# Performance work log

Hardware: AMD Instinct MI355X
Metric: run time of the kernel (lower is better)

The kernel has to match this reference:

```python
import jax, jax.numpy as jnp
import numpy as np

HEADS = 16  # matches init_kwargs


def setup_inputs() -> dict:
    key = jax.random.key(0)
    ks = jax.random.split(key, 9)
    N, L, E, D = 2, 2048, 1024, 64
    return {
        "query": jax.random.normal(ks[0], (N, L, E), dtype=jnp.float32),
        "keys": jax.random.normal(ks[1], (N, L, E), dtype=jnp.float32),
        "values": jax.random.normal(ks[2], (N, L, E), dtype=jnp.float32),
        "masks": jax.random.randint(ks[3], (N, 1, 1, L), 0, 2, dtype=jnp.int32),
        "Wq": jax.random.normal(ks[4], (D, D), dtype=jnp.float32) / np.sqrt(D),
        "Wk": jax.random.normal(ks[5], (D, D), dtype=jnp.float32) / np.sqrt(D),
        "Wv": jax.random.normal(ks[6], (D, D), dtype=jnp.float32) / np.sqrt(D),
        "Wo": jax.random.normal(ks[7], (E, E), dtype=jnp.float32) / np.sqrt(E),
        "bo": jax.random.normal(ks[8], (E,), dtype=jnp.float32),
    }


def reference(query, keys, values, masks, Wq, Wk, Wv, Wo, bo):
    N, Lq, E = query.shape
    Lk = keys.shape[1]
    H = HEADS
    D = E // H
    # split heads: [N, L, H, D]
    q = query.reshape(N, Lq, H, D)
    k = keys.reshape(N, Lk, H, D)
    v = values.reshape(N, Lk, H, D)
    # per-head linear projections (weights shared across heads); Linear: x @ W.T
    q = jnp.einsum("nqhd,ed->nqhe", q, Wq)
    k = jnp.einsum("nkhd,ed->nkhe", k, Wk)
    v = jnp.einsum("nkhd,ed->nkhe", v, Wv)
    # scores [N, H, Lq, Lk]
    scores = jnp.einsum("nqhd,nkhd->nhqk", q, k)
    scores = jnp.where(masks == 0, jnp.float32(-1e20), scores)
    # NOTE: original scales by sqrt(embed_size), not sqrt(head_dim)
    attn = jax.nn.softmax(scores / jnp.sqrt(jnp.float32(E)), axis=3)
    out = jnp.einsum("nhqk,nkhd->nqhd", attn, v).reshape(N, Lq, E)
    return out @ Wo.T + bo
```

## Files before the change

kernel.cpp:

```cpp
#include <hip/hip_runtime.h>


typedef __bf16 bf16_t;
typedef __bf16 bf16x4 __attribute__((ext_vector_type(4)));
typedef __bf16 bf16x8 __attribute__((ext_vector_type(8)));
typedef float f32x4 __attribute__((ext_vector_type(4)));
typedef unsigned int u32x4 __attribute__((ext_vector_type(4)));

#define MFMA16(a, b, c) __builtin_amdgcn_mfma_f32_16x16x32_bf16((a), (b), (c), 0, 0, 0)

#define GLOAD_LDS16(gp, lp)                                              \
    __builtin_amdgcn_global_load_lds(                                    \
        (const __attribute__((address_space(1))) void*)(gp),             \
        (__attribute__((address_space(3))) void*)(lp), 16, 0, 0)

__device__ inline bf16x8 cvt8(const float* __restrict__ p, float scale) {
    f32x4 a = *(const f32x4*)p;
    f32x4 b = *(const f32x4*)(p + 4);
    bf16x8 r;
    r[0] = (bf16_t)(a[0] * scale); r[1] = (bf16_t)(a[1] * scale);
    r[2] = (bf16_t)(a[2] * scale); r[3] = (bf16_t)(a[3] * scale);
    r[4] = (bf16_t)(b[0] * scale); r[5] = (bf16_t)(b[1] * scale);
    r[6] = (bf16_t)(b[2] * scale); r[7] = (bf16_t)(b[3] * scale);
    return r;
}

__device__ inline bf16x8 cvt8s(const f32x4 a, const f32x4 b, float scale) {
    bf16x8 r;
    r[0] = (bf16_t)(a[0] * scale); r[1] = (bf16_t)(a[1] * scale);
    r[2] = (bf16_t)(a[2] * scale); r[3] = (bf16_t)(a[3] * scale);
    r[4] = (bf16_t)(b[0] * scale); r[5] = (bf16_t)(b[1] * scale);
    r[6] = (bf16_t)(b[2] * scale); r[7] = (bf16_t)(b[3] * scale);
    return r;
}

__device__ inline float exp2_fast(float x) {
    float r;
    asm("v_exp_f32 %0, %1" : "=v"(r) : "v"(x));
    return r;
}

__device__ inline unsigned cvt_pk_bf16(float lo, float hi) {
    unsigned r;
    asm("v_cvt_pk_bf16_f32 %0, %1, %2" : "=v"(r) : "v"(lo), "v"(hi));
    return r;
}

__device__ inline void xchg_quads(unsigned &x, unsigned &y) {
    asm("v_permlane32_swap_b32 %0, %1\n\t"
        "v_permlane16_swap_b32 %0, %1"
        : "+v"(x), "+v"(y));
}

__global__ __launch_bounds__(256) void scan_kernel(const int* __restrict__ msk,
                                                   int* __restrict__ excl,
                                                   int* __restrict__ lmap)
{
    __shared__ int wsum[4];
    const int n = blockIdx.x;
    const int t = threadIdx.x, lane = t & 63, w = t >> 6;
    const int* m = msk + n * 2048;
    int* e = excl + n * 2049;
    int* lm = lmap + n * 2048;

    int v[8], s = 0;
    #pragma unroll
    for (int j = 0; j < 8; j++) { v[j] = (m[t * 8 + j] != 0); s += v[j]; }

    int inc = s;
    #pragma unroll
    for (int d = 1; d < 64; d <<= 1) {
        int o = __shfl_up(inc, d);
        if (lane >= d) inc += o;
    }
    if (lane == 63) wsum[w] = inc;
    __syncthreads();
    int off = 0;
    #pragma unroll
    for (int i = 0; i < 4; i++)
        if (i < w) off += wsum[i];

    int a = off + inc - s;
    #pragma unroll
    for (int j = 0; j < 8; j++) {
        e[t * 8 + j] = a;
        if (v[j]) lm[a] = t * 8 + j;
        a += v[j];
    }
    if (t == 255) e[2048] = a;
}

__global__ __launch_bounds__(256) void qkv_proj_kernel(
    const float* __restrict__ qin, const float* __restrict__ kin,
    const float* __restrict__ vin,
    const float* __restrict__ Wq, const float* __restrict__ Wk,
    const float* __restrict__ Wv, const float* __restrict__ Wo,
    const int* __restrict__ excl, const int* __restrict__ lmap,
    bf16_t* __restrict__ qp, bf16_t* __restrict__ kc, bf16_t* __restrict__ vcT,
    bf16_t* __restrict__ Wob)
{
    __shared__ __align__(16) char smem[51200];

    const int t = threadIdx.x;
    const int w = t >> 6, lane = t & 63, quad = lane >> 4, l16 = lane & 15;

    if (blockIdx.y == 3) {
        int idx = blockIdx.x * 1024 + t * 4;
        f32x4 v = *(const f32x4*)&Wo[idx];
        bf16x4 r;
        r[0] = (bf16_t)v[0]; r[1] = (bf16_t)v[1];
        r[2] = (bf16_t)v[2]; r[3] = (bf16_t)v[3];
        *(bf16x4*)&Wob[idx] = r;
        return;
    }

    if (blockIdx.y == 2) {
        bf16_t* Ct = (bf16_t*)smem;
        const int h = blockIdx.x & 15;
        const int ctile = blockIdx.x >> 4;
        const int n = ctile >> 5;
        const int c0 = (ctile & 31) * 64;
        const int Lc = excl[n * 2049 + 2048];
        if (c0 >= Lc) return;

        const int p0 = w * 16 + l16;
        int cs = c0 + p0; if (cs > Lc - 1) cs = Lc - 1;
        const int tg = lmap[n * 2048 + cs];
        const size_t rb = ((size_t)(n * 2048 + tg)) * 1024 + h * 64;

        bf16x8 b0 = cvt8(&vin[rb + quad * 8], 1.0f);
        bf16x8 b1 = cvt8(&vin[rb + 32 + quad * 8], 1.0f);

        #pragma unroll
        for (int nt = 0; nt < 4; nt++) {
            bf16x8 a0 = cvt8(&Wv[(nt * 16 + l16) * 64 + quad * 8], 1.0f);
            bf16x8 a1 = cvt8(&Wv[(nt * 16 + l16) * 64 + 32 + quad * 8], 1.0f);
            f32x4 acc = {0.f, 0.f, 0.f, 0.f};
            acc = MFMA16(a0, b0, acc);
            acc = MFMA16(a1, b1, acc);
            #pragma unroll
            for (int r = 0; r < 4; r++)
                Ct[(nt * 16 + quad * 4 + r) * 72 + w * 16 + l16] = (bf16_t)acc[r];
        }
        __syncthreads();
        const int p = t & 63, rg = t >> 6;
        const int cnt = (Lc - c0 < 64) ? (Lc - c0) : 64;
        if (p < cnt) {
            size_t ob = ((size_t)(n * 16 + h)) * 131072 + c0 + p;
            #pragma unroll
            for (int rr = 0; rr < 16; rr++) {
                int r = rg * 16 + rr;
                vcT[ob + (size_t)r * 2048] = Ct[r * 72 + p];
            }
        }
        return;
    }

    if (blockIdx.x >= 512) return;
    const bool isK = (blockIdx.y == 1);
    const float* x; const float* W; float scale;
    int n = 0, c0 = 0, Lc = 0;
    if (!isK) { x = qin; W = Wq; scale = 0.04508422f; }
    else {
        x = kin; W = Wk; scale = 1.0f;
        n = blockIdx.x >> 8;
        c0 = (blockIdx.x & 255) * 8;
        Lc = excl[n * 2049 + 2048];
        if (c0 >= Lc) return;
    }

    float* Xs = (float*)smem;
    bf16_t* Ct2 = (bf16_t*)(smem + 32768);

    const int g0 = blockIdx.x * 128;

    #pragma unroll
    for (int j = 0; j < 8; j++) {
        int br = w * 32 + j * 4;
        int srow = br + (lane >> 4);
        int scol = ((lane & 15) ^ (srow & 15)) * 4;
        size_t gaddr;
        if (!isK) {
            gaddr = (size_t)(g0 + srow) * 64 + scol;
        } else {
            int csx = c0 + (srow >> 4); if (csx > Lc - 1) csx = Lc - 1;
            int hs = srow & 15;
            int ls = lmap[n * 2048 + csx];
            gaddr = ((size_t)((n * 2048 + ls) * 16 + hs)) * 64 + scol;
        }
        GLOAD_LDS16(&x[gaddr], &Xs[br * 64]);
    }
    __syncthreads();

    const int rbase = w * 32;
    bf16x8 a[2][2];
    #pragma unroll
    for (int qs = 0; qs < 2; qs++) {
        int row = rbase + qs * 16 + l16;
        const char* rowp = (const char*)Xs + (size_t)row * 256;
        int swb = (row & 15) << 4;
        #pragma unroll
        for (int c = 0; c < 2; c++) {
            f32x4 lo = *(const f32x4*)(rowp + ((c * 128 + quad * 32) ^ swb));
            f32x4 hi = *(const f32x4*)(rowp + ((c * 128 + quad * 32 + 16) ^ swb));
            a[qs][c] = cvt8s(lo, hi, scale);
        }
    }

    f32x4 acc[4][2];
    #pragma unroll
    for (int nt = 0; nt < 4; nt++) {
        bf16x8 b0 = cvt8(&W[(nt * 16 + l16) * 64 + quad * 8], 1.0f);
        bf16x8 b1 = cvt8(&W[(nt * 16 + l16) * 64 + 32 + quad * 8], 1.0f);
        #pragma unroll
        for (int qs = 0; qs < 2; qs++) {
            f32x4 z = {0.f, 0.f, 0.f, 0.f};
            z = MFMA16(a[qs][0], b0, z);
            z = MFMA16(a[qs][1], b1, z);
            acc[nt][qs] = z;
        }
    }

    #pragma unroll
    for (int nt = 0; nt < 4; nt++)
        #pragma unroll
        for (int qs = 0; qs < 2; qs++)
            #pragma unroll
            for (int r = 0; r < 4; r++)
                Ct2[(rbase + qs * 16 + quad * 4 + r) * 72 + nt * 16 + l16] = (bf16_t)acc[nt][qs][r];
    __syncthreads();

    #pragma unroll
    for (int it = 0; it < 4; it++) {
        int j = it * 32 + (t >> 3);
        bf16x8 val = *(const bf16x8*)&Ct2[j * 72 + (t & 7) * 8];
        if (isK) {
            int c = c0 + (j >> 4), h2 = j & 15;
            if (c < Lc)
                *(bf16x8*)&kc[(((size_t)(n * 16 + h2)) * 2048 + c) * 64 + (t & 7) * 8] = val;
        } else {
            int g = g0 + j, h2 = g & 15, token = g >> 4;
            int n2 = token >> 11, l = token & 2047;
            *(bf16x8*)&qp[(((size_t)(n2 * 16 + h2)) * 2048 + l) * 64 + (t & 7) * 8] = val;
        }
    }
}

__global__ __launch_bounds__(256) void attn_kernel(
    const bf16_t* __restrict__ qp, const bf16_t* __restrict__ kc,
    const bf16_t* __restrict__ vcT, const int* __restrict__ excl,
    bf16_t* __restrict__ ao)
{
    __shared__ bf16_t Kt[2][128][64];
    __shared__ bf16_t Vt[2][64][128];

    const int t = threadIdx.x;
    const int w = t >> 6, lane = t & 63, quad = lane >> 4, l16 = lane & 15;

    const int flat = blockIdx.x;
    const int xcd = flat & 7, slot = flat >> 3;
    const int nh = xcd * 4 + (slot >> 4), qb = slot & 15;
    const int n = nh >> 4, h = nh & 15;
    const int qbase = qb * 128 + w * 32;
    const size_t nhbase = (size_t)nh * 131072;

    const int Lc = excl[n * 2049 + 2048];
    const int ntiles = (Lc + 127) >> 7;

    const int ksrow = lane >> 3;
    const int kscol = ((lane & 7) ^ (lane >> 3)) * 8;
    const int swr = l16 & 7;
    const int ck0 = (quad ^ swr) * 8;
    const int ck1 = ((quad + 4) ^ swr) * 8;

    bf16x8 aq[2][2];
    #pragma unroll
    for (int qs = 0; qs < 2; qs++)
        #pragma unroll
        for (int c = 0; c < 2; c++)
            aq[qs][c] = *(const bf16x8*)&qp[nhbase + (size_t)(qbase + qs * 16 + l16) * 64 + c * 32 + quad * 8];

    f32x4 o[2][4];
    float lsum[2] = {0.f, 0.f};
    #pragma unroll
    for (int qs = 0; qs < 2; qs++)
        #pragma unroll
        for (int dt = 0; dt < 4; dt++) {
            o[qs][dt][0] = 0.f; o[qs][dt][1] = 0.f; o[qs][dt][2] = 0.f; o[qs][dt][3] = 0.f;
        }

#define STAGE_KV(buf, kn)                                                     \
    {                                                                         \
        _Pragma("unroll")                                                     \
        for (int j = 0; j < 4; j++) {                                         \
            int rb = w * 32 + j * 8;                                          \
            GLOAD_LDS16(&kc[nhbase + (size_t)((kn) + rb + ksrow) * 64 + kscol],\
                        &Kt[buf][rb][0]);                                     \
        }                                                                     \
        _Pragma("unroll")                                                     \
        for (int j = 0; j < 4; j++) {                                         \
            int rb = w * 16 + j * 4;                                          \
            int d = rb + (lane >> 4);                                         \
            int sc = ((lane & 15) ^ (d & 15)) * 8;                            \
            GLOAD_LDS16(&vcT[nhbase + (size_t)d * 2048 + (kn) + sc],          \
                        &Vt[buf][rb][0]);                                     \
        }                                                                     \
    }

    STAGE_KV(0, 0);

    for (int i = 0; i < ntiles; i++) {
        const int cb = i & 1, nb = cb ^ 1;
        const int k0 = i * 128;
        __syncthreads();

        if (i + 1 < ntiles) STAGE_KV(nb, k0 + 128);

        #pragma unroll
        for (int hf = 0; hf < 2; hf++) {
            const int kh = k0 + hf * 64;

            f32x4 st[2][4];
            __builtin_amdgcn_s_setprio(1);
            #pragma unroll
            for (int ct = 0; ct < 4; ct++) {
                bf16x8 kb0 = *(const bf16x8*)&Kt[cb][hf * 64 + ct * 16 + l16][ck0];
                bf16x8 kb1 = *(const bf16x8*)&Kt[cb][hf * 64 + ct * 16 + l16][ck1];
                #pragma unroll
                for (int qs = 0; qs < 2; qs++) {
                    f32x4 acc = {0.f, 0.f, 0.f, 0.f};
                    acc = MFMA16(kb0, aq[qs][0], acc);
                    acc = MFMA16(kb1, aq[qs][1], acc);
                    st[qs][ct] = acc;
                }
            }
            __builtin_amdgcn_s_setprio(0);

            if (kh + 64 <= Lc) {
                #pragma unroll
                for (int qs = 0; qs < 2; qs++)
                    #pragma unroll
                    for (int ct = 0; ct < 4; ct++)
                        #pragma unroll
                        for (int r = 0; r < 4; r++) {
                            float p = exp2_fast(st[qs][ct][r]);
                            lsum[qs] += p;
                            st[qs][ct][r] = p;
                        }
            } else {
                #pragma unroll
                for (int qs = 0; qs < 2; qs++)
                    #pragma unroll
                    for (int ct = 0; ct < 4; ct++)
                        #pragma unroll
                        for (int r = 0; r < 4; r++) {
                            int kk = kh + ct * 16 + quad * 4 + r;
                            float p = (kk < Lc) ? exp2_fast(st[qs][ct][r]) : 0.0f;
                            lsum[qs] += p;
                            st[qs][ct][r] = p;
                        }
            }

            bf16x8 bp[2][2];
            #pragma unroll
            for (int qs = 0; qs < 2; qs++) {
                unsigned u[4][2];
                #pragma unroll
                for (int ct = 0; ct < 4; ct++) {
                    u[ct][0] = cvt_pk_bf16(st[qs][ct][0], st[qs][ct][1]);
                    u[ct][1] = cvt_pk_bf16(st[qs][ct][2], st[qs][ct][3]);
                }
                #pragma unroll
                for (int hh = 0; hh < 2; hh++) {
                    unsigned b0 = u[2 * hh][0], b2 = u[2 * hh + 1][0];
                    xchg_quads(b0, b2);
                    unsigned b1 = u[2 * hh][1], b3 = u[2 * hh + 1][1];
                    xchg_quads(b1, b3);
                    u32x4 q4 = {b0, b1, b2, b3};
                    bp[qs][hh] = __builtin_bit_cast(bf16x8, q4);
                }
            }

            __builtin_amdgcn_s_setprio(1);
            #pragma unroll
            for (int dt = 0; dt < 4; dt++) {
                bf16x8 va0 = *(const bf16x8*)&Vt[cb][dt * 16 + l16][((hf * 8 + quad) ^ l16) * 8];
                bf16x8 va1 = *(const bf16x8*)&Vt[cb][dt * 16 + l16][((hf * 8 + 4 + quad) ^ l16) * 8];
                #pragma unroll
                for (int qs = 0; qs < 2; qs++) {
                    o[qs][dt] = MFMA16(va0, bp[qs][0], o[qs][dt]);
                    o[qs][dt] = MFMA16(va1, bp[qs][1], o[qs][dt]);
                }
            }
            __builtin_amdgcn_s_setprio(0);
        }
    }

    #pragma unroll
    for (int qs = 0; qs < 2; qs++) {
        float v = lsum[qs];
        v += __shfl_xor(v, 16);
        v += __shfl_xor(v, 32);
        float inv = 1.0f / v;
        const int q = qbase + qs * 16 + l16;
        const size_t base = ((size_t)n * 2048 + q) * 1024 + h * 64;
        #pragma unroll
        for (int dt = 0; dt < 4; dt++) {
            bf16x4 ov;
            #pragma unroll
            for (int r = 0; r < 4; r++) ov[r] = (bf16_t)(o[qs][dt][r] * inv);
            *(bf16x4*)&ao[base + dt * 16 + quad * 4] = ov;
        }
    }
}

__global__ __launch_bounds__(256, 2) void out_proj_kernel(
    const bf16_t* __restrict__ X, const bf16_t* __restrict__ Wob,
    const float* __restrict__ bo, float* __restrict__ out)
{
    __shared__ bf16_t Xs[2][128][64];
    __shared__ bf16_t Ws[2][64][64];

    const int t = threadIdx.x;
    const int w = t >> 6, lane = t & 63, quad = lane >> 4, l16 = lane & 15;
    const int Mbase = blockIdx.x * 128;
    const int Nbase = blockIdx.y * 64;
    const int mrow = (w & 1) * 64;
    const int ncol = (w >> 1) * 32;

    const int scol = ((lane & 7) ^ (lane >> 3)) * 8;
    const int swr  = l16 & 7;

    f32x4 acc[4][2];
    #pragma unroll
    for (int mi = 0; mi < 4; mi++)
        #pragma unroll
        for (int ni = 0; ni < 2; ni++) {
            acc[mi][ni][0] = 0.f; acc[mi][ni][1] = 0.f;
            acc[mi][ni][2] = 0.f; acc[mi][ni][3] = 0.f;
        }

    #pragma unroll
    for (int j = 0; j < 4; j++) {
        int br = w * 32 + j * 8;
        GLOAD_LDS16(&X[(size_t)(Mbase + br + (lane >> 3)) * 1024 + scol], &Xs[0][br][0]);
    }
    #pragma unroll
    for (int j = 0; j < 2; j++) {
        int br = w * 16 + j * 8;
        GLOAD_LDS16(&Wob[(size_t)(Nbase + br + (lane >> 3)) * 1024 + scol], &Ws[0][br][0]);
    }

    for (int i = 0; i < 16; i++) {
        const int cb = i & 1, nb = cb ^ 1;
        __syncthreads();

        if (i < 15) {
            const int kn = (i + 1) * 64;
            #pragma unroll
            for (int j = 0; j < 4; j++) {
                int br = w * 32 + j * 8;
                GLOAD_LDS16(&X[(size_t)(Mbase + br + (lane >> 3)) * 1024 + kn + scol],
                            &Xs[nb][br][0]);
            }
            #pragma unroll
            for (int j = 0; j < 2; j++) {
                int br = w * 16 + j * 8;
                GLOAD_LDS16(&Wob[(size_t)(Nbase + br + (lane >> 3)) * 1024 + kn + scol],
                            &Ws[nb][br][0]);
            }
        }

        #pragma unroll
        for (int c = 0; c < 2; c++) {
            bf16x8 bfr[2];
            #pragma unroll
            for (int ni = 0; ni < 2; ni++)
                bfr[ni] = *(const bf16x8*)&Ws[cb][ncol + ni * 16 + l16][((c * 4 + quad) ^ swr) * 8];
            #pragma unroll
            for (int mi = 0; mi < 4; mi++) {
                bf16x8 afr = *(const bf16x8*)&Xs[cb][mrow + mi * 16 + l16][((c * 4 + quad) ^ swr) * 8];
                #pragma unroll
                for (int ni = 0; ni < 2; ni++)
                    acc[mi][ni] = MFMA16(afr, bfr[ni], acc[mi][ni]);
            }
        }
    }

    #pragma unroll
    for (int ni = 0; ni < 2; ni++) {
        float b = bo[Nbase + ncol + ni * 16 + l16];
        #pragma unroll
        for (int mi = 0; mi < 4; mi++) {
            #pragma unroll
            for (int r = 0; r < 4; r++) {
                int row = Mbase + mrow + mi * 16 + quad * 4 + r;
                out[(size_t)row * 1024 + Nbase + ncol + ni * 16 + l16] = acc[mi][ni][r] + b;
            }
        }
    }
}

extern "C" void kernel_launch(void* const* d_in, const int* in_sizes, int n_in,
                              void* d_out, int out_size, void* d_ws, size_t ws_size,
                              hipStream_t stream)
{
    const float* qin = (const float*)d_in[0];
    const float* kin = (const float*)d_in[1];
    const float* vin = (const float*)d_in[2];
    const int*   msk = (const int*)d_in[3];
    const float* Wq  = (const float*)d_in[4];
    const float* Wk  = (const float*)d_in[5];
    const float* Wv  = (const float*)d_in[6];
    const float* Wo  = (const float*)d_in[7];
    const float* bo  = (const float*)d_in[8];
    float* out = (float*)d_out;

    bf16_t* ws  = (bf16_t*)d_ws;
    bf16_t* qp  = ws;
    bf16_t* kc  = ws + 4194304;
    bf16_t* vcT = ws + 8388608;
    bf16_t* ao  = ws + 12582912;
    bf16_t* Wob = ws + 16777216;
    int* excl   = (int*)(ws + 17825792);
    int* lmap   = excl + 4100;

    scan_kernel<<<2, 256, 0, stream>>>(msk, excl, lmap);
    qkv_proj_kernel<<<dim3(1024, 4), 256, 0, stream>>>(qin, kin, vin, Wq, Wk, Wv, Wo,
                                                        excl, lmap, qp, kc, vcT, Wob);
    attn_kernel<<<dim3(512), 256, 0, stream>>>(qp, kc, vcT, excl, ao);
    out_proj_kernel<<<dim3(32, 16), 256, 0, stream>>>(ao, Wob, bo, out);
}
```

Measured before the change: 167.0 us.

## Pre-convert projection weights to bf16 and widen out-proj N tile

Converts Wq (with the softmax scale folded in), Wk and Wv to bf16 once, in extra blocks of the scan kernel. The QKV projection blocks then load bf16 weights directly instead of converting fp32 in every block, and the Q activation scaling is removed. The output projection tile grows from 128x64 to 128x128 per block, which halves the grid and doubles the accumulators per thread. That improves operand reuse but costs more registers and LDS, and leaves fewer blocks to fill the GPU.

```diff
diff --git a/kernel.cpp b/kernel.cpp
--- a/kernel.cpp
+++ b/kernel.cpp
@@ -14,23 +14,23 @@
         (const __attribute__((address_space(1))) void*)(gp),             \
         (__attribute__((address_space(3))) void*)(lp), 16, 0, 0)
 
-__device__ inline bf16x8 cvt8(const float* __restrict__ p, float scale) {
+__device__ inline bf16x8 cvt8(const float* __restrict__ p) {
     f32x4 a = *(const f32x4*)p;
     f32x4 b = *(const f32x4*)(p + 4);
     bf16x8 r;
-    r[0] = (bf16_t)(a[0] * scale); r[1] = (bf16_t)(a[1] * scale);
-    r[2] = (bf16_t)(a[2] * scale); r[3] = (bf16_t)(a[3] * scale);
-    r[4] = (bf16_t)(b[0] * scale); r[5] = (bf16_t)(b[1] * scale);
-    r[6] = (bf16_t)(b[2] * scale); r[7] = (bf16_t)(b[3] * scale);
+    r[0] = (bf16_t)a[0]; r[1] = (bf16_t)a[1];
+    r[2] = (bf16_t)a[2]; r[3] = (bf16_t)a[3];
+    r[4] = (bf16_t)b[0]; r[5] = (bf16_t)b[1];
+    r[6] = (bf16_t)b[2]; r[7] = (bf16_t)b[3];
     return r;
 }
 
-__device__ inline bf16x8 cvt8s(const f32x4 a, const f32x4 b, float scale) {
+__device__ inline bf16x8 cvt8s(const f32x4 a, const f32x4 b) {
     bf16x8 r;
-    r[0] = (bf16_t)(a[0] * scale); r[1] = (bf16_t)(a[1] * scale);
-    r[2] = (bf16_t)(a[2] * scale); r[3] = (bf16_t)(a[3] * scale);
-    r[4] = (bf16_t)(b[0] * scale); r[5] = (bf16_t)(b[1] * scale);
-    r[6] = (bf16_t)(b[2] * scale); r[7] = (bf16_t)(b[3] * scale);
+    r[0] = (bf16_t)a[0]; r[1] = (bf16_t)a[1];
+    r[2] = (bf16_t)a[2]; r[3] = (bf16_t)a[3];
+    r[4] = (bf16_t)b[0]; r[5] = (bf16_t)b[1];
+    r[6] = (bf16_t)b[2]; r[7] = (bf16_t)b[3];
     return r;
 }
 
@@ -52,13 +52,34 @@
         : "+v"(x), "+v"(y));
 }
 
-__global__ __launch_bounds__(256) void scan_kernel(const int* __restrict__ msk,
-                                                   int* __restrict__ excl,
-                                                   int* __restrict__ lmap)
+__global__ __launch_bounds__(256) void scan_kernel(
+    const int* __restrict__ msk, int* __restrict__ excl, int* __restrict__ lmap,
+    const float* __restrict__ Wq, const float* __restrict__ Wk,
+    const float* __restrict__ Wv,
+    bf16_t* __restrict__ Wqb, bf16_t* __restrict__ Wkb, bf16_t* __restrict__ Wvb)
 {
+    const int t = threadIdx.x;
+
+    if (blockIdx.x >= 2) {
+        const int wi = blockIdx.x - 2;
+        const float* Ws = (wi == 0) ? Wq : (wi == 1) ? Wk : Wv;
+        bf16_t* Wb = (wi == 0) ? Wqb : (wi == 1) ? Wkb : Wvb;
+        const float scale = (wi == 0) ? 0.04508422f : 1.0f;
+        #pragma unroll
+        for (int j = 0; j < 4; j++) {
+            int idx = t * 16 + j * 4;
+            f32x4 v = *(const f32x4*)&Ws[idx];
+            bf16x4 r;
+            r[0] = (bf16_t)(v[0] * scale); r[1] = (bf16_t)(v[1] * scale);
+            r[2] = (bf16_t)(v[2] * scale); r[3] = (bf16_t)(v[3] * scale);
+            *(bf16x4*)&Wb[idx] = r;
+        }
+        return;
+    }
+
     __shared__ int wsum[4];
     const int n = blockIdx.x;
-    const int t = threadIdx.x, lane = t & 63, w = t >> 6;
+    const int lane = t & 63, w = t >> 6;
     const int* m = msk + n * 2048;
     int* e = excl + n * 2049;
     int* lm = lmap + n * 2048;
@@ -93,8 +114,8 @@
 __global__ __launch_bounds__(256) void qkv_proj_kernel(
     const float* __restrict__ qin, const float* __restrict__ kin,
     const float* __restrict__ vin,
-    const float* __restrict__ Wq, const float* __restrict__ Wk,
-    const float* __restrict__ Wv, const float* __restrict__ Wo,
+    const bf16_t* __restrict__ Wqb, const bf16_t* __restrict__ Wkb,
+    const bf16_t* __restrict__ Wvb, const float* __restrict__ Wo,
     const int* __restrict__ excl, const int* __restrict__ lmap,
     bf16_t* __restrict__ qp, bf16_t* __restrict__ kc, bf16_t* __restrict__ vcT,
     bf16_t* __restrict__ Wob)
@@ -128,13 +149,13 @@
         const int tg = lmap[n * 2048 + cs];
         const size_t rb = ((size_t)(n * 2048 + tg)) * 1024 + h * 64;
 
-        bf16x8 b0 = cvt8(&vin[rb + quad * 8], 1.0f);
-        bf16x8 b1 = cvt8(&vin[rb + 32 + quad * 8], 1.0f);
+        bf16x8 b0 = cvt8(&vin[rb + quad * 8]);
+        bf16x8 b1 = cvt8(&vin[rb + 32 + quad * 8]);
 
         #pragma unroll
         for (int nt = 0; nt < 4; nt++) {
-            bf16x8 a0 = cvt8(&Wv[(nt * 16 + l16) * 64 + quad * 8], 1.0f);
-            bf16x8 a1 = cvt8(&Wv[(nt * 16 + l16) * 64 + 32 + quad * 8], 1.0f);
+            bf16x8 a0 = *(const bf16x8*)&Wvb[(nt * 16 + l16) * 64 + quad * 8];
+            bf16x8 a1 = *(const bf16x8*)&Wvb[(nt * 16 + l16) * 64 + 32 + quad * 8];
             f32x4 acc = {0.f, 0.f, 0.f, 0.f};
             acc = MFMA16(a0, b0, acc);
             acc = MFMA16(a1, b1, acc);
@@ -158,11 +179,11 @@
 
     if (blockIdx.x >= 512) return;
     const bool isK = (blockIdx.y == 1);
-    const float* x; const float* W; float scale;
+    const float* x; const bf16_t* Wb;
     int n = 0, c0 = 0, Lc = 0;
-    if (!isK) { x = qin; W = Wq; scale = 0.04508422f; }
+    if (!isK) { x = qin; Wb = Wqb; }
     else {
-        x = kin; W = Wk; scale = 1.0f;
+        x = kin; Wb = Wkb;
         n = blockIdx.x >> 8;
         c0 = (blockIdx.x & 255) * 8;
         Lc = excl[n * 2049 + 2048];
@@ -203,15 +224,15 @@
         for (int c = 0; c < 2; c++) {
             f32x4 lo = *(const f32x4*)(rowp + ((c * 128 + quad * 32) ^ swb));
             f32x4 hi = *(const f32x4*)(rowp + ((c * 128 + quad * 32 + 16) ^ swb));
-            a[qs][c] = cvt8s(lo, hi, scale);
+            a[qs][c] = cvt8s(lo, hi);
         }
     }
 
     f32x4 acc[4][2];
     #pragma unroll
     for (int nt = 0; nt < 4; nt++) {
-        bf16x8 b0 = cvt8(&W[(nt * 16 + l16) * 64 + quad * 8], 1.0f);
-        bf16x8 b1 = cvt8(&W[(nt * 16 + l16) * 64 + 32 + quad * 8], 1.0f);
+        bf16x8 b0 = *(const bf16x8*)&Wb[(nt * 16 + l16) * 64 + quad * 8];
+        bf16x8 b1 = *(const bf16x8*)&Wb[(nt * 16 + l16) * 64 + 32 + quad * 8];
         #pragma unroll
         for (int qs = 0; qs < 2; qs++) {
             f32x4 z = {0.f, 0.f, 0.f, 0.f};
@@ -419,23 +440,23 @@
     const float* __restrict__ bo, float* __restrict__ out)
 {
     __shared__ bf16_t Xs[2][128][64];
-    __shared__ bf16_t Ws[2][64][64];
+    __shared__ bf16_t Ws[2][128][64];
 
     const int t = threadIdx.x;
     const int w = t >> 6, lane = t & 63, quad = lane >> 4, l16 = lane & 15;
     const int Mbase = blockIdx.x * 128;
-    const int Nbase = blockIdx.y * 64;
+    const int Nbase = blockIdx.y * 128;
     const int mrow = (w & 1) * 64;
-    const int ncol = (w >> 1) * 32;
+    const int ncol = (w >> 1) * 64;
 
     const int scol = ((lane & 7) ^ (lane >> 3)) * 8;
     const int swr  = l16 & 7;
 
-    f32x4 acc[4][2];
+    f32x4 acc[4][4];
     #pragma unroll
     for (int mi = 0; mi < 4; mi++)
         #pragma unroll
-        for (int ni = 0; ni < 2; ni++) {
+        for (int ni = 0; ni < 4; ni++) {
             acc[mi][ni][0] = 0.f; acc[mi][ni][1] = 0.f;
             acc[mi][ni][2] = 0.f; acc[mi][ni][3] = 0.f;
         }
@@ -444,10 +465,6 @@
     for (int j = 0; j < 4; j++) {
         int br = w * 32 + j * 8;
         GLOAD_LDS16(&X[(size_t)(Mbase + br + (lane >> 3)) * 1024 + scol], &Xs[0][br][0]);
-    }
-    #pragma unroll
-    for (int j = 0; j < 2; j++) {
-        int br = w * 16 + j * 8;
         GLOAD_LDS16(&Wob[(size_t)(Nbase + br + (lane >> 3)) * 1024 + scol], &Ws[0][br][0]);
     }
 
@@ -462,10 +479,6 @@
                 int br = w * 32 + j * 8;
                 GLOAD_LDS16(&X[(size_t)(Mbase + br + (lane >> 3)) * 1024 + kn + scol],
                             &Xs[nb][br][0]);
-            }
-            #pragma unroll
-            for (int j = 0; j < 2; j++) {
-                int br = w * 16 + j * 8;
                 GLOAD_LDS16(&Wob[(size_t)(Nbase + br + (lane >> 3)) * 1024 + kn + scol],
                             &Ws[nb][br][0]);
             }
@@ -473,22 +486,22 @@
 
         #pragma unroll
         for (int c = 0; c < 2; c++) {
-            bf16x8 bfr[2];
-            #pragma unroll
-            for (int ni = 0; ni < 2; ni++)
+            bf16x8 bfr[4];
+            #pragma unroll
+            for (int ni = 0; ni < 4; ni++)
                 bfr[ni] = *(const bf16x8*)&Ws[cb][ncol + ni * 16 + l16][((c * 4 + quad) ^ swr) * 8];
             #pragma unroll
             for (int mi = 0; mi < 4; mi++) {
                 bf16x8 afr = *(const bf16x8*)&Xs[cb][mrow + mi * 16 + l16][((c * 4 + quad) ^ swr) * 8];
                 #pragma unroll
-                for (int ni = 0; ni < 2; ni++)
+                for (int ni = 0; ni < 4; ni++)
                     acc[mi][ni] = MFMA16(afr, bfr[ni], acc[mi][ni]);
             }
         }
     }
 
     #pragma unroll
-    for (int ni = 0; ni < 2; ni++) {
+    for (int ni = 0; ni < 4; ni++) {
         float b = bo[Nbase + ncol + ni * 16 + l16];
         #pragma unroll
         for (int mi = 0; mi < 4; mi++) {
@@ -524,10 +537,13 @@
     bf16_t* Wob = ws + 16777216;
     int* excl   = (int*)(ws + 17825792);
     int* lmap   = excl + 4100;
-
-    scan_kernel<<<2, 256, 0, stream>>>(msk, excl, lmap);
-    qkv_proj_kernel<<<dim3(1024, 4), 256, 0, stream>>>(qin, kin, vin, Wq, Wk, Wv, Wo,
+    bf16_t* Wqb = (bf16_t*)(lmap + 4096);
+    bf16_t* Wkb = Wqb + 4096;
+    bf16_t* Wvb = Wkb + 4096;
+
+    scan_kernel<<<5, 256, 0, stream>>>(msk, excl, lmap, Wq, Wk, Wv, Wqb, Wkb, Wvb);
+    qkv_proj_kernel<<<dim3(1024, 4), 256, 0, stream>>>(qin, kin, vin, Wqb, Wkb, Wvb, Wo,
                                                         excl, lmap, qp, kc, vcT, Wob);
     attn_kernel<<<dim3(512), 256, 0, stream>>>(qp, kc, vcT, excl, ao);
-    out_proj_kernel<<<dim3(32, 16), 256, 0, stream>>>(ao, Wob, bo, out);
-}
+    out_proj_kernel<<<dim3(32, 8), 256, 0, stream>>>(ao, Wob, bo, out);
+}
```

Measured after the change: 165.7 us. No clear change (-0.8%).
